# Optimization experiments

Measured on AMD Instinct MI355X. Metric: run time of the kernel, lower is better.

## Reference

```python
import jax, jax.numpy as jnp
import numpy as np

B_SZ, SEQ, H, P, N, LBLK = 16, 2048, 16, 64, 16, 64  # batch, seqlen, heads, d_head, d_state, block_len


def setup_inputs() -> dict:
    key = jax.random.key(0)
    k1, k2, k3, k4 = jax.random.split(key, 4)
    X = jax.random.normal(k1, (B_SZ, SEQ, H, P), jnp.float32)
    # A is a per-step log-decay; real Mamba2 has A < 0 so exp(segsum) stays bounded
    A = -0.1 * jax.random.uniform(k2, (B_SZ, SEQ, H), jnp.float32)
    B = jax.random.normal(k3, (B_SZ, SEQ, H, N), jnp.float32)
    C = jax.random.normal(k4, (B_SZ, SEQ, H, N), jnp.float32)
    return {"X": X, "A": A, "B": B, "C": C}


def _exp_segsum(x):
    """x: (..., t). Returns exp(cumsum[i]-cumsum[j]) for j<=i, 0 above diagonal."""
    t = x.shape[-1]
    cs = jnp.cumsum(x, axis=-1)
    diff = cs[..., :, None] - cs[..., None, :]
    mask = jnp.tril(jnp.ones((t, t), dtype=bool))
    return jnp.where(mask, jnp.exp(jnp.where(mask, diff, 0.0)), 0.0)


def ssd_forward(X, A, B, C):
    b, s, h, p = X.shape
    n = B.shape[-1]
    c = s // LBLK
    # chunk: (b, c, l, h, *)
    Xb = X.reshape(b, c, LBLK, h, p)
    Bb = B.reshape(b, c, LBLK, h, n)
    Cb = C.reshape(b, c, LBLK, h, n)
    Ab = jnp.transpose(A.reshape(b, c, LBLK, h), (0, 3, 1, 2))  # (b, h, c, l)
    A_cs = jnp.cumsum(Ab, axis=-1)                               # (b, h, c, l)

    # 1. intra-chunk (diagonal block) output: kernel 1
    L = _exp_segsum(Ab)                                          # (b, h, c, l, s)
    CB = jnp.einsum("bclhn,bcshn->bhcls", Cb, Bb)               # (b, h, c, l, s)
    Y_diag = jnp.einsum("bhcls,bcshp->bclhp", CB * L, Xb)

    # 2. per-chunk end states: kernel 2
    decay_states = jnp.exp(A_cs[..., -1:] - A_cs)                # (b, h, c, l)
    states = jnp.einsum("bclhn,bhcl,bclhp->bchpn", Bb, decay_states, Xb)

    # 3. inter-chunk recurrence (zero initial state): kernel 3
    states = jnp.concatenate([jnp.zeros_like(states[:, :1]), states], axis=1)  # (b, c+1, h, p, n)
    A_last_pad = jnp.pad(A_cs[..., -1], ((0, 0), (0, 0), (1, 0)))              # (b, h, c+1)
    decay_chunk = _exp_segsum(A_last_pad)                                       # (b, h, c+1, c+1)
    new_states = jnp.einsum("bhzc,bchpn->bzhpn", decay_chunk, states)
    states_in = new_states[:, :-1]                                              # (b, c, h, p, n)

    # 4. off-diagonal (state -> output) contribution: kernel 4
    Y_off = jnp.einsum("bclhn,bchpn,bhcl->bclhp", Cb, states_in, jnp.exp(A_cs))

    return (Y_diag + Y_off).reshape(b, s, h, p)


def reference(X, A, B, C):
    return ssd_forward(X, A, B, C)
```

## Files before the change

kernel.cpp:

```cpp
#include <hip/hip_runtime.h>

#define BS 16
#define SEQL 2048
#define NH 16
#define PD 64
#define ND 16
#define LB 64
#define NC 32

typedef __attribute__((ext_vector_type(8))) short bf16x8;
typedef __attribute__((ext_vector_type(4))) float f32x4;

static __device__ __forceinline__ unsigned short f2bf(float x) {
  unsigned int u = __float_as_uint(x);
  unsigned int r = (u + 0x7FFFu + ((u >> 16) & 1u)) >> 16;
  return (unsigned short)r;
}

__global__ __launch_bounds__(512, 2) void ssd_fused(
    const float* __restrict__ Xg, const float* __restrict__ Ag,
    const float* __restrict__ Bg, const float* __restrict__ Cg,
    float* __restrict__ Yg) {
  const int h = blockIdx.x & (NH - 1);
  const int b = blockIdx.x >> 4;
  const int t = threadIdx.x;
  const int w = t >> 6;
  const int lane = t & 63;
  const int g = lane >> 4;
  const int cc = lane & 15;

  __shared__ __align__(16) unsigned short sXt[PD][LB + 8];
  __shared__ __align__(16) unsigned short sM [LB][LB + 8];
  __shared__ __align__(16) unsigned short sB [LB][ND + 8];
  __shared__ __align__(16) unsigned short sC [LB][ND + 8];
  __shared__ __align__(16) unsigned short sBdT[ND][LB + 8];
  __shared__ __align__(16) float          sSTf[2][PD][ND + 4];
  __shared__ __align__(16) unsigned short sSTb[2][PD][ND + 8];

  for (int i = t; i < PD * (ND + 4); i += 512) ((float*)sSTf[0])[i] = 0.f;
  for (int i = t; i < PD * (ND + 8); i += 512) ((unsigned short*)sSTb[0])[i] = 0;

  const int xl0 = (t >> 4) * 2, xp0 = (t & 15) * 4;
  const int bl  = t >> 3,       bn0 = (t & 7) * 2;
  float4 px0, px1; float2 pb2, pc2; float pa;

#define PREF(cc_) do { \
    const size_t s0_ = (size_t)(b * SEQL + (cc_) * LB); \
    px0 = *(const float4*)&Xg[(s0_ + xl0) * (NH * PD) + h * PD + xp0]; \
    px1 = *(const float4*)&Xg[(s0_ + xl0 + 1) * (NH * PD) + h * PD + xp0]; \
    pb2 = *(const float2*)&Bg[(s0_ + bl) * (NH * ND) + h * ND + bn0]; \
    pc2 = *(const float2*)&Cg[(s0_ + bl) * (NH * ND) + h * ND + bn0]; \
    pa  = Ag[(s0_ + lane) * NH + h]; \
  } while (0)

  PREF(0);

  for (int c = 0; c < NC; ++c) {
    float v = pa;
#pragma unroll
    for (int d = 1; d < 64; d <<= 1) {
      float o = __shfl_up(v, d, 64);
      if (lane >= d) v += o;
    }
    const float acs = v;
    const float er = expf(acs);
    const float rr = expf(-acs);
    const float etot = __shfl(er, 63);

    {
#pragma unroll
      for (int j = 0; j < 4; ++j) {
        const float xa = (&px0.x)[j], xb = (&px1.x)[j];
        *(unsigned int*)&sXt[xp0 + j][xl0] =
            (unsigned int)f2bf(xa) | ((unsigned int)f2bf(xb) << 16);
      }
      const float el = __shfl(er, bl);
      const float dl = etot * __shfl(rr, bl);
      *(unsigned int*)&sB[bl][bn0] =
          (unsigned int)f2bf(pb2.x) | ((unsigned int)f2bf(pb2.y) << 16);
      *(unsigned int*)&sC[bl][bn0] =
          (unsigned int)f2bf(el * pc2.x) | ((unsigned int)f2bf(el * pc2.y) << 16);
      sBdT[bn0][bl]     = f2bf(dl * pb2.x);
      sBdT[bn0 + 1][bl] = f2bf(dl * pb2.y);
    }
    if (c + 1 < NC) PREF(c + 1);
    __syncthreads();

    {
      const int lb1 = w & 3;
      const int l = lb1 * 16 + cc;
      bf16x8 zf = {0, 0, 0, 0, 0, 0, 0, 0};
      bf16x8 cf = zf;
      if (g < 2) cf = *(const bf16x8*)&sC[l][g * 8];
#pragma unroll
      for (int ii = 0; ii < 2; ++ii) {
        const int sb = (w < 4 ? 0 : 2) + ii;
        uint2 out = make_uint2(0u, 0u);
        if (sb <= lb1) {
          bf16x8 bfr = zf;
          if (g < 2) bfr = *(const bf16x8*)&sB[sb * 16 + cc][g * 8];
          f32x4 z4 = {0.f, 0.f, 0.f, 0.f};
          f32x4 d = __builtin_amdgcn_mfma_f32_16x16x32_bf16(bfr, cf, z4, 0, 0, 0);
          float m[4];
#pragma unroll
          for (int r = 0; r < 4; ++r) {
            const int srow = sb * 16 + 4 * g + r;
            m[r] = d[r] * __shfl(rr, srow);
            if (sb == lb1 && (4 * g + r) > cc) m[r] = 0.f;
          }
          out.x = (unsigned int)f2bf(m[0]) | ((unsigned int)f2bf(m[1]) << 16);
          out.y = (unsigned int)f2bf(m[2]) | ((unsigned int)f2bf(m[3]) << 16);
        }
        *(uint2*)&sM[l][sb * 16 + g * 4] = out;
      }
    }
    __syncthreads();

    const int cur = c & 1, nxt = cur ^ 1;
    if (w < 4) {
      const int lb = w;
      const int l = lb * 16 + cc;
      bf16x8 zf = {0, 0, 0, 0, 0, 0, 0, 0};
      bf16x8 cf = zf;
      if (g < 2) cf = *(const bf16x8*)&sC[l][g * 8];
      bf16x8 a0 = *(const bf16x8*)&sM[l][g * 8];
      bf16x8 a1 = zf;
      if (lb >= 2) a1 = *(const bf16x8*)&sM[l][32 + g * 8];
#pragma unroll
      for (int pb = 0; pb < 4; ++pb) {
        const int p = pb * 16 + cc;
        bf16x8 stf = zf;
        if (g < 2) stf = *(const bf16x8*)&sSTb[cur][p][g * 8];
        f32x4 acc = {0.f, 0.f, 0.f, 0.f};
        acc = __builtin_amdgcn_mfma_f32_16x16x32_bf16(cf, stf, acc, 0, 0, 0);
        bf16x8 xf0 = *(const bf16x8*)&sXt[p][g * 8];
        acc = __builtin_amdgcn_mfma_f32_16x16x32_bf16(a0, xf0, acc, 0, 0, 0);
        if (lb >= 2) {
          bf16x8 xf1 = *(const bf16x8*)&sXt[p][32 + g * 8];
          acc = __builtin_amdgcn_mfma_f32_16x16x32_bf16(a1, xf1, acc, 0, 0, 0);
        }
        const size_t yb =
            ((size_t)(b * SEQL + c * LB + lb * 16 + 4 * g)) * (NH * PD) + h * PD + p;
#pragma unroll
        for (int r = 0; r < 4; ++r)
          Yg[yb + (size_t)r * (NH * PD)] = acc[r];
      }
    } else {
      const int pb = w - 4;
      const int p = pb * 16 + cc;
      bf16x8 ad0 = *(const bf16x8*)&sBdT[cc][g * 8];
      bf16x8 ad1 = *(const bf16x8*)&sBdT[cc][32 + g * 8];
      bf16x8 xt0 = *(const bf16x8*)&sXt[p][g * 8];
      bf16x8 xt1 = *(const bf16x8*)&sXt[p][32 + g * 8];
      f32x4 acc = {0.f, 0.f, 0.f, 0.f};
      acc = __builtin_amdgcn_mfma_f32_16x16x32_bf16(ad0, xt0, acc, 0, 0, 0);
      acc = __builtin_amdgcn_mfma_f32_16x16x32_bf16(ad1, xt1, acc, 0, 0, 0);
      float4 old = *(const float4*)&sSTf[cur][p][4 * g];
      float4 nw;
      nw.x = old.x * etot + acc[0];
      nw.y = old.y * etot + acc[1];
      nw.z = old.z * etot + acc[2];
      nw.w = old.w * etot + acc[3];
      *(float4*)&sSTf[nxt][p][4 * g] = nw;
      uint2 ub;
      ub.x = (unsigned int)f2bf(nw.x) | ((unsigned int)f2bf(nw.y) << 16);
      ub.y = (unsigned int)f2bf(nw.z) | ((unsigned int)f2bf(nw.w) << 16);
      *(uint2*)&sSTb[nxt][p][4 * g] = ub;
    }
    __syncthreads();
  }
#undef PREF
}

extern "C" void kernel_launch(void* const* d_in, const int* in_sizes, int n_in,
                              void* d_out, int out_size, void* d_ws, size_t ws_size,
                              hipStream_t stream) {
  (void)in_sizes; (void)n_in; (void)out_size; (void)d_ws; (void)ws_size;
  const float* X = (const float*)d_in[0];
  const float* A = (const float*)d_in[1];
  const float* B = (const float*)d_in[2];
  const float* C = (const float*)d_in[3];
  float* Y = (float*)d_out;
  ssd_fused<<<BS * NH, 512, 0, stream>>>(X, A, B, C, Y);
}
```

Before: 79.88 us.

## Pipeline chunk staging across iterations and rebalance per-chunk work across waves

Restructures the chunk loop so the next chunk's cumsum and shared-memory staging run at the end of the current iteration into a double-buffered, XOR-swizzled X tile. Each iteration now needs two barriers instead of three. The causal M tiles are spread over all 8 waves, and the Y output is split so every wave computes two P-blocks. The transposed B-decay tile is loaded with a separate strided global read, so it can be written with packed stores instead of scalar ones. In exchange the kernel uses more registers, extra global loads of B, and a custom barrier that waits only on lgkmcnt, and the launch-bounds occupancy hint is dropped.

Measured after the change: 93.42 us. +17.0%, slower.

```diff
diff --git a/kernel.cpp b/kernel.cpp
--- a/kernel.cpp
+++ b/kernel.cpp
@@ -7,17 +7,26 @@
 #define ND 16
 #define LB 64
 #define NC 32
+#define NHP (NH * PD)
+#define NHN (NH * ND)
 
 typedef __attribute__((ext_vector_type(8))) short bf16x8;
 typedef __attribute__((ext_vector_type(4))) float f32x4;
 
 static __device__ __forceinline__ unsigned short f2bf(float x) {
   unsigned int u = __float_as_uint(x);
-  unsigned int r = (u + 0x7FFFu + ((u >> 16) & 1u)) >> 16;
-  return (unsigned short)r;
-}
-
-__global__ __launch_bounds__(512, 2) void ssd_fused(
+  return (unsigned short)((u + 0x7FFFu + ((u >> 16) & 1u)) >> 16);
+}
+static __device__ __forceinline__ unsigned int pk2(float a, float b) {
+  return (unsigned int)f2bf(a) | ((unsigned int)f2bf(b) << 16);
+}
+static __device__ __forceinline__ void barrier_lgkm() {
+  asm volatile("s_waitcnt lgkmcnt(0)" ::: "memory");
+  __builtin_amdgcn_s_barrier();
+  asm volatile("" ::: "memory");
+}
+
+__global__ __launch_bounds__(512) void ssd_fused(
     const float* __restrict__ Xg, const float* __restrict__ Ag,
     const float* __restrict__ Bg, const float* __restrict__ Cg,
     float* __restrict__ Yg) {
@@ -29,147 +38,176 @@
   const int g = lane >> 4;
   const int cc = lane & 15;
 
-  __shared__ __align__(16) unsigned short sXt[PD][LB + 8];
-  __shared__ __align__(16) unsigned short sM [LB][LB + 8];
-  __shared__ __align__(16) unsigned short sB [LB][ND + 8];
-  __shared__ __align__(16) unsigned short sC [LB][ND + 8];
+  __shared__ __align__(16) unsigned short sXt[2][PD][64];
+  __shared__ __align__(16) unsigned short sM[LB][LB + 8];
+  __shared__ __align__(16) unsigned short sB[LB][ND + 8];
+  __shared__ __align__(16) unsigned short sC[LB][ND + 8];
   __shared__ __align__(16) unsigned short sBdT[ND][LB + 8];
-  __shared__ __align__(16) float          sSTf[2][PD][ND + 4];
+  __shared__ __align__(16) float sSTf[2][PD][ND + 4];
   __shared__ __align__(16) unsigned short sSTb[2][PD][ND + 8];
+
+  const int xp0 = (t & 15) * 4, xl0 = (t >> 4) * 2;
+  const int bl = t >> 3, bn0 = (t & 7) * 2;
+  const int n_bt = t >> 5, l_bt = (t & 31) * 2;
+
+  const int lb1 = (int)((0x33222110u >> (4 * w)) & 0xFu);
+  const int sb1 = (int)((0x20210100u >> (4 * w)) & 0xFu);
+
+  float4 px0, px1;
+  float2 pb2, pc2;
+  float pbA_v, pbB_v, pa;
+  float er, rr, etot, er_n, rr_n, etot_n;
+
+#define PREF(ci) do { \
+    const size_t s0_ = (size_t)(b * SEQL + (ci) * LB); \
+    px0 = *(const float4*)&Xg[(s0_ + xl0) * NHP + h * PD + xp0]; \
+    px1 = *(const float4*)&Xg[(s0_ + xl0 + 1) * NHP + h * PD + xp0]; \
+    pb2 = *(const float2*)&Bg[(s0_ + bl) * NHN + h * ND + bn0]; \
+    pc2 = *(const float2*)&Cg[(s0_ + bl) * NHN + h * ND + bn0]; \
+    pbA_v = Bg[(s0_ + l_bt) * NHN + h * ND + n_bt]; \
+    pbB_v = Bg[(s0_ + l_bt + 1) * NHN + h * ND + n_bt]; \
+    pa = Ag[(s0_ + lane) * NH + h]; \
+  } while (0)
+
+#define CUMSUM_STAGE(bufi) do { \
+    float v_ = pa; \
+    _Pragma("unroll") \
+    for (int d_ = 1; d_ < 64; d_ <<= 1) { \
+      float o_ = __shfl_up(v_, d_, 64); \
+      if (lane >= d_) v_ += o_; \
+    } \
+    er_n = expf(v_); rr_n = expf(-v_); etot_n = __shfl(er_n, 63); \
+    _Pragma("unroll") \
+    for (int j_ = 0; j_ < 4; ++j_) { \
+      const int p_ = xp0 + j_; \
+      const int idx_ = (((xl0 >> 3) ^ ((p_ >> 3) & 7)) << 3) | (xl0 & 7); \
+      *(unsigned int*)&sXt[bufi][p_][idx_] = pk2((&px0.x)[j_], (&px1.x)[j_]); \
+    } \
+    { const float el_ = __shfl(er_n, bl); \
+      *(unsigned int*)&sB[bl][bn0] = pk2(pb2.x, pb2.y); \
+      *(unsigned int*)&sC[bl][bn0] = pk2(el_ * pc2.x, el_ * pc2.y); } \
+    { const float d0_ = etot_n * __shfl(rr_n, l_bt); \
+      const float d1_ = etot_n * __shfl(rr_n, l_bt + 1); \
+      *(unsigned int*)&sBdT[n_bt][l_bt] = pk2(d0_ * pbA_v, d1_ * pbB_v); } \
+  } while (0)
+
+  const bf16x8 zf8 = {0, 0, 0, 0, 0, 0, 0, 0};
+
+  auto xfrag = [&](int buf, int p_, int l0_) -> bf16x8 {
+    const int idx_ = (((l0_ >> 3) ^ ((p_ >> 3) & 7)) << 3);
+    return *(const bf16x8*)&sXt[buf][p_][idx_];
+  };
+
+  auto p1tile = [&](int lb_, int sb_) {
+    const int l_ = lb_ * 16 + cc;
+    bf16x8 cf = zf8, bfr = zf8;
+    if (g < 2) {
+      cf = *(const bf16x8*)&sC[l_][g * 8];
+      bfr = *(const bf16x8*)&sB[sb_ * 16 + cc][g * 8];
+    }
+    f32x4 z4 = {0.f, 0.f, 0.f, 0.f};
+    f32x4 d = __builtin_amdgcn_mfma_f32_16x16x32_bf16(bfr, cf, z4, 0, 0, 0);
+    float mm[4];
+#pragma unroll
+    for (int r = 0; r < 4; ++r) {
+      const int srow = sb_ * 16 + 4 * g + r;
+      mm[r] = d[r] * __shfl(rr, srow);
+      if (sb_ == lb_ && (4 * g + r) > cc) mm[r] = 0.f;
+    }
+    uint2 o;
+    o.x = pk2(mm[0], mm[1]);
+    o.y = pk2(mm[2], mm[3]);
+    *(uint2*)&sM[l_][sb_ * 16 + g * 4] = o;
+  };
 
   for (int i = t; i < PD * (ND + 4); i += 512) ((float*)sSTf[0])[i] = 0.f;
   for (int i = t; i < PD * (ND + 8); i += 512) ((unsigned short*)sSTb[0])[i] = 0;
-
-  const int xl0 = (t >> 4) * 2, xp0 = (t & 15) * 4;
-  const int bl  = t >> 3,       bn0 = (t & 7) * 2;
-  float4 px0, px1; float2 pb2, pc2; float pa;
-
-#define PREF(cc_) do { \
-    const size_t s0_ = (size_t)(b * SEQL + (cc_) * LB); \
-    px0 = *(const float4*)&Xg[(s0_ + xl0) * (NH * PD) + h * PD + xp0]; \
-    px1 = *(const float4*)&Xg[(s0_ + xl0 + 1) * (NH * PD) + h * PD + xp0]; \
-    pb2 = *(const float2*)&Bg[(s0_ + bl) * (NH * ND) + h * ND + bn0]; \
-    pc2 = *(const float2*)&Cg[(s0_ + bl) * (NH * ND) + h * ND + bn0]; \
-    pa  = Ag[(s0_ + lane) * NH + h]; \
-  } while (0)
-
   PREF(0);
+  CUMSUM_STAGE(0);
+  er = er_n; rr = rr_n; etot = etot_n;
+  PREF(1);
+  barrier_lgkm();
+
+  const int lbY = w & 3;
+  const int pbb = (w < 4) ? 0 : 2;
+  const int pS = (w - 4) * 16 + cc;
 
   for (int c = 0; c < NC; ++c) {
-    float v = pa;
-#pragma unroll
-    for (int d = 1; d < 64; d <<= 1) {
-      float o = __shfl_up(v, d, 64);
-      if (lane >= d) v += o;
-    }
-    const float acs = v;
-    const float er = expf(acs);
-    const float rr = expf(-acs);
-    const float etot = __shfl(er, 63);
+    const int cur = c & 1, nxt = cur ^ 1;
+
+    p1tile(lb1, sb1);
+    if (w >= 6) p1tile(lb1, sb1 + 1);
+    if (w == 4) *(uint2*)&sM[cc][16 + g * 4] = make_uint2(0u, 0u);
+    if (w == 5) *(uint2*)&sM[32 + cc][48 + g * 4] = make_uint2(0u, 0u);
+
+    bf16x8 cfY = zf8;
+    if (g < 2) cfY = *(const bf16x8*)&sC[lbY * 16 + cc][g * 8];
+    bf16x8 stf[2], xfa[2], xfb[2];
+#pragma unroll
+    for (int pbi = 0; pbi < 2; ++pbi) {
+      const int p_ = (pbb + pbi) * 16 + cc;
+      stf[pbi] = zf8;
+      if (g < 2) stf[pbi] = *(const bf16x8*)&sSTb[cur][p_][g * 8];
+      xfa[pbi] = xfrag(cur, p_, g * 8);
+      xfb[pbi] = zf8;
+      if (lbY >= 2) xfb[pbi] = xfrag(cur, p_, 32 + g * 8);
+    }
+    bf16x8 ad0 = zf8, ad1 = zf8, xt0 = zf8, xt1 = zf8;
+    float4 stold = make_float4(0.f, 0.f, 0.f, 0.f);
+    if (w >= 4) {
+      ad0 = *(const bf16x8*)&sBdT[cc][g * 8];
+      ad1 = *(const bf16x8*)&sBdT[cc][32 + g * 8];
+      xt0 = xfrag(cur, pS, g * 8);
+      xt1 = xfrag(cur, pS, 32 + g * 8);
+      stold = *(const float4*)&sSTf[cur][pS][4 * g];
+    }
+
+    barrier_lgkm();
 
     {
-#pragma unroll
-      for (int j = 0; j < 4; ++j) {
-        const float xa = (&px0.x)[j], xb = (&px1.x)[j];
-        *(unsigned int*)&sXt[xp0 + j][xl0] =
-            (unsigned int)f2bf(xa) | ((unsigned int)f2bf(xb) << 16);
+      const int lY = lbY * 16 + cc;
+      bf16x8 a0 = *(const bf16x8*)&sM[lY][g * 8];
+      bf16x8 a1 = zf8;
+      if (lbY >= 2) a1 = *(const bf16x8*)&sM[lY][32 + g * 8];
+#pragma unroll
+      for (int pbi = 0; pbi < 2; ++pbi) {
+        const int p_ = (pbb + pbi) * 16 + cc;
+        f32x4 acc = {0.f, 0.f, 0.f, 0.f};
+        acc = __builtin_amdgcn_mfma_f32_16x16x32_bf16(cfY, stf[pbi], acc, 0, 0, 0);
+        acc = __builtin_amdgcn_mfma_f32_16x16x32_bf16(a0, xfa[pbi], acc, 0, 0, 0);
+        if (lbY >= 2)
+          acc = __builtin_amdgcn_mfma_f32_16x16x32_bf16(a1, xfb[pbi], acc, 0, 0, 0);
+        const size_t yb =
+            ((size_t)(b * SEQL + c * LB + lbY * 16 + 4 * g)) * NHP + h * PD + p_;
+#pragma unroll
+        for (int r = 0; r < 4; ++r) Yg[yb + (size_t)r * NHP] = acc[r];
       }
-      const float el = __shfl(er, bl);
-      const float dl = etot * __shfl(rr, bl);
-      *(unsigned int*)&sB[bl][bn0] =
-          (unsigned int)f2bf(pb2.x) | ((unsigned int)f2bf(pb2.y) << 16);
-      *(unsigned int*)&sC[bl][bn0] =
-          (unsigned int)f2bf(el * pc2.x) | ((unsigned int)f2bf(el * pc2.y) << 16);
-      sBdT[bn0][bl]     = f2bf(dl * pb2.x);
-      sBdT[bn0 + 1][bl] = f2bf(dl * pb2.y);
-    }
-    if (c + 1 < NC) PREF(c + 1);
-    __syncthreads();
-
-    {
-      const int lb1 = w & 3;
-      const int l = lb1 * 16 + cc;
-      bf16x8 zf = {0, 0, 0, 0, 0, 0, 0, 0};
-      bf16x8 cf = zf;
-      if (g < 2) cf = *(const bf16x8*)&sC[l][g * 8];
-#pragma unroll
-      for (int ii = 0; ii < 2; ++ii) {
-        const int sb = (w < 4 ? 0 : 2) + ii;
-        uint2 out = make_uint2(0u, 0u);
-        if (sb <= lb1) {
-          bf16x8 bfr = zf;
-          if (g < 2) bfr = *(const bf16x8*)&sB[sb * 16 + cc][g * 8];
-          f32x4 z4 = {0.f, 0.f, 0.f, 0.f};
-          f32x4 d = __builtin_amdgcn_mfma_f32_16x16x32_bf16(bfr, cf, z4, 0, 0, 0);
-          float m[4];
-#pragma unroll
-          for (int r = 0; r < 4; ++r) {
-            const int srow = sb * 16 + 4 * g + r;
-            m[r] = d[r] * __shfl(rr, srow);
-            if (sb == lb1 && (4 * g + r) > cc) m[r] = 0.f;
-          }
-          out.x = (unsigned int)f2bf(m[0]) | ((unsigned int)f2bf(m[1]) << 16);
-          out.y = (unsigned int)f2bf(m[2]) | ((unsigned int)f2bf(m[3]) << 16);
-        }
-        *(uint2*)&sM[l][sb * 16 + g * 4] = out;
-      }
-    }
-    __syncthreads();
-
-    const int cur = c & 1, nxt = cur ^ 1;
-    if (w < 4) {
-      const int lb = w;
-      const int l = lb * 16 + cc;
-      bf16x8 zf = {0, 0, 0, 0, 0, 0, 0, 0};
-      bf16x8 cf = zf;
-      if (g < 2) cf = *(const bf16x8*)&sC[l][g * 8];
-      bf16x8 a0 = *(const bf16x8*)&sM[l][g * 8];
-      bf16x8 a1 = zf;
-      if (lb >= 2) a1 = *(const bf16x8*)&sM[l][32 + g * 8];
-#pragma unroll
-      for (int pb = 0; pb < 4; ++pb) {
-        const int p = pb * 16 + cc;
-        bf16x8 stf = zf;
-        if (g < 2) stf = *(const bf16x8*)&sSTb[cur][p][g * 8];
-        f32x4 acc = {0.f, 0.f, 0.f, 0.f};
-        acc = __builtin_amdgcn_mfma_f32_16x16x32_bf16(cf, stf, acc, 0, 0, 0);
-        bf16x8 xf0 = *(const bf16x8*)&sXt[p][g * 8];
-        acc = __builtin_amdgcn_mfma_f32_16x16x32_bf16(a0, xf0, acc, 0, 0, 0);
-        if (lb >= 2) {
-          bf16x8 xf1 = *(const bf16x8*)&sXt[p][32 + g * 8];
-          acc = __builtin_amdgcn_mfma_f32_16x16x32_bf16(a1, xf1, acc, 0, 0, 0);
-        }
-        const size_t yb =
-            ((size_t)(b * SEQL + c * LB + lb * 16 + 4 * g)) * (NH * PD) + h * PD + p;
-#pragma unroll
-        for (int r = 0; r < 4; ++r)
-          Yg[yb + (size_t)r * (NH * PD)] = acc[r];
-      }
-    } else {
-      const int pb = w - 4;
-      const int p = pb * 16 + cc;
-      bf16x8 ad0 = *(const bf16x8*)&sBdT[cc][g * 8];
-      bf16x8 ad1 = *(const bf16x8*)&sBdT[cc][32 + g * 8];
-      bf16x8 xt0 = *(const bf16x8*)&sXt[p][g * 8];
-      bf16x8 xt1 = *(const bf16x8*)&sXt[p][32 + g * 8];
-      f32x4 acc = {0.f, 0.f, 0.f, 0.f};
-      acc = __builtin_amdgcn_mfma_f32_16x16x32_bf16(ad0, xt0, acc, 0, 0, 0);
-      acc = __builtin_amdgcn_mfma_f32_16x16x32_bf16(ad1, xt1, acc, 0, 0, 0);
-      float4 old = *(const float4*)&sSTf[cur][p][4 * g];
+    }
+    if (w >= 4) {
+      f32x4 s4 = {0.f, 0.f, 0.f, 0.f};
+      s4 = __builtin_amdgcn_mfma_f32_16x16x32_bf16(ad0, xt0, s4, 0, 0, 0);
+      s4 = __builtin_amdgcn_mfma_f32_16x16x32_bf16(ad1, xt1, s4, 0, 0, 0);
       float4 nw;
-      nw.x = old.x * etot + acc[0];
-      nw.y = old.y * etot + acc[1];
-      nw.z = old.z * etot + acc[2];
-      nw.w = old.w * etot + acc[3];
-      *(float4*)&sSTf[nxt][p][4 * g] = nw;
+      nw.x = stold.x * etot + s4[0];
+      nw.y = stold.y * etot + s4[1];
+      nw.z = stold.z * etot + s4[2];
+      nw.w = stold.w * etot + s4[3];
+      *(float4*)&sSTf[nxt][pS][4 * g] = nw;
       uint2 ub;
-      ub.x = (unsigned int)f2bf(nw.x) | ((unsigned int)f2bf(nw.y) << 16);
-      ub.y = (unsigned int)f2bf(nw.z) | ((unsigned int)f2bf(nw.w) << 16);
-      *(uint2*)&sSTb[nxt][p][4 * g] = ub;
-    }
-    __syncthreads();
+      ub.x = pk2(nw.x, nw.y);
+      ub.y = pk2(nw.z, nw.w);
+      *(uint2*)&sSTb[nxt][pS][4 * g] = ub;
+    }
+    if (c + 1 < NC) {
+      CUMSUM_STAGE(nxt);
+      if (c + 2 < NC) PREF(c + 2);
+      er = er_n; rr = rr_n; etot = etot_n;
+    }
+
+    barrier_lgkm();
   }
 #undef PREF
+#undef CUMSUM_STAGE
 }
 
 extern "C" void kernel_launch(void* const* d_in, const int* in_sizes, int n_in,
```
